# Kernel optimization log

Measured on AMD Instinct MI355X. Metric: run time of the kernel, lower is better.

Reference implementation:

```python
import jax, jax.numpy as jnp
import numpy as np
from jax import lax

T, D, NH, CATS = 1024, 2048, 2048, 1000


def setup_inputs() -> dict:
    key = jax.random.key(0)
    ks = jax.random.split(key, 16)
    s = 0.02
    return {
        "x": jax.random.normal(ks[0], (T, D), dtype=jnp.float32),
        "Wh": jax.random.normal(ks[1], (NH, D), dtype=jnp.float32) * s,
        "Wz": jax.random.normal(ks[2], (NH, D), dtype=jnp.float32) * s,
        "Wr": jax.random.normal(ks[3], (NH, D), dtype=jnp.float32) * s,
        "Uh": jax.random.normal(ks[4], (NH, NH), dtype=jnp.float32) * s,
        "Uz": jax.random.normal(ks[5], (NH, NH), dtype=jnp.float32) * s,
        "bz": jax.random.normal(ks[6], (NH,), dtype=jnp.float32) * s,
        "Ur": jax.random.normal(ks[7], (NH, NH), dtype=jnp.float32) * s,
        "br": jax.random.normal(ks[8], (NH,), dtype=jnp.float32) * s,
        "Wout": jax.random.normal(ks[9], (CATS, NH), dtype=jnp.float32) * s,
        "h0": jax.random.normal(ks[10], (NH,), dtype=jnp.float32),
        "zt0": jax.random.normal(ks[11], (NH,), dtype=jnp.float32),
        "htilde0": jax.random.normal(ks[12], (NH,), dtype=jnp.float32),
        "hprev0": jax.random.normal(ks[13], (NH,), dtype=jnp.float32),
    }


def reference(x, Wh, Wz, Wr, Uh, Uz, bz, Ur, br, Wout, h0, zt0, htilde0, hprev0):
    # Batch the input projections over all timesteps: [T,d] @ [d,nh] -> [T,nh]
    xh = x @ Wh.T
    xz = x @ Wz.T
    xr = x @ Wr.T

    # Faithful to the original update ORDER: h is computed from the *stale*
    # zt/htilde (from the previous iteration), then gates are refreshed.
    # The original's hadamard(a, b) = linear(a, diag(b)) is exactly a * b.
    def step(carry, xs):
        h, zt, htilde, hprev = carry
        xh_t, xz_t, xr_t = xs
        h_new = (1.0 - zt) * hprev + zt * htilde
        zt_new = jax.nn.sigmoid(xz_t + hprev @ Uz.T + bz)
        htilde_new = jnp.tanh(xh_t + hprev @ Uh.T)
        # rt = sigmoid(xr_t + hprev @ Ur.T + br)  # computed in original, never used
        return (h_new, zt_new, htilde_new, h_new), None

    (h_fin, _, _, _), _ = lax.scan(step, (h0, zt0, htilde0, hprev0), (xh, xz, xr))
    logits = h_fin @ Wout.T  # [cats]
    return jax.nn.softmax(logits, axis=0)
```

## Files before the change

### kernel.cpp

```cpp
#include <hip/hip_runtime.h>
#include <math.h>

#define TT  1024
#define DD  2048
#define NHH 2048
#define CC  1000

__global__ void k_init(const float* __restrict__ hp0, unsigned long long* __restrict__ Hbuf) {
    int i = blockIdx.x * blockDim.x + threadIdx.x;
    if (i < NHH) Hbuf[i] = (unsigned long long)__float_as_uint(hp0[i]);
}

__global__ __launch_bounds__(256) void k_gemm(const float* __restrict__ X,
                                              const float* __restrict__ Wh,
                                              const float* __restrict__ Wz,
                                              const float* __restrict__ bz,
                                              float* __restrict__ XH,
                                              float* __restrict__ XZ) {
    __shared__ float As[32][68];
    __shared__ float Bs[32][68];
    const int z = blockIdx.z;
    const float* __restrict__ W = z ? Wz : Wh;
    float* __restrict__ OUT = z ? XZ : XH;
    const int n0 = blockIdx.x * 64;
    const int m0 = blockIdx.y * 64;
    const int tid = threadIdx.x;
    const int tx = tid & 15, ty = tid >> 4;
    const int lr = tid >> 2;
    const int lc = (tid & 3) * 8;

    float acc[4][4] = {};
    for (int k0 = 0; k0 < DD; k0 += 32) {
        float4 a0 = *(const float4*)&X[(size_t)(m0 + lr) * DD + k0 + lc];
        float4 a1 = *(const float4*)&X[(size_t)(m0 + lr) * DD + k0 + lc + 4];
        float4 b0 = *(const float4*)&W[(size_t)(n0 + lr) * DD + k0 + lc];
        float4 b1 = *(const float4*)&W[(size_t)(n0 + lr) * DD + k0 + lc + 4];
        As[lc+0][lr]=a0.x; As[lc+1][lr]=a0.y; As[lc+2][lr]=a0.z; As[lc+3][lr]=a0.w;
        As[lc+4][lr]=a1.x; As[lc+5][lr]=a1.y; As[lc+6][lr]=a1.z; As[lc+7][lr]=a1.w;
        Bs[lc+0][lr]=b0.x; Bs[lc+1][lr]=b0.y; Bs[lc+2][lr]=b0.z; Bs[lc+3][lr]=b0.w;
        Bs[lc+4][lr]=b1.x; Bs[lc+5][lr]=b1.y; Bs[lc+6][lr]=b1.z; Bs[lc+7][lr]=b1.w;
        __syncthreads();
#pragma unroll
        for (int kk = 0; kk < 32; ++kk) {
            float4 av = *(const float4*)&As[kk][ty * 4];
            float4 bv = *(const float4*)&Bs[kk][tx * 4];
            acc[0][0] = fmaf(av.x, bv.x, acc[0][0]); acc[0][1] = fmaf(av.x, bv.y, acc[0][1]);
            acc[0][2] = fmaf(av.x, bv.z, acc[0][2]); acc[0][3] = fmaf(av.x, bv.w, acc[0][3]);
            acc[1][0] = fmaf(av.y, bv.x, acc[1][0]); acc[1][1] = fmaf(av.y, bv.y, acc[1][1]);
            acc[1][2] = fmaf(av.y, bv.z, acc[1][2]); acc[1][3] = fmaf(av.y, bv.w, acc[1][3]);
            acc[2][0] = fmaf(av.z, bv.x, acc[2][0]); acc[2][1] = fmaf(av.z, bv.y, acc[2][1]);
            acc[2][2] = fmaf(av.z, bv.z, acc[2][2]); acc[2][3] = fmaf(av.z, bv.w, acc[2][3]);
            acc[3][0] = fmaf(av.w, bv.x, acc[3][0]); acc[3][1] = fmaf(av.w, bv.y, acc[3][1]);
            acc[3][2] = fmaf(av.w, bv.z, acc[3][2]); acc[3][3] = fmaf(av.w, bv.w, acc[3][3]);
        }
        __syncthreads();
    }
    float4 bias = make_float4(0.f, 0.f, 0.f, 0.f);
    if (z) bias = *(const float4*)&bz[n0 + tx * 4];
#pragma unroll
    for (int i = 0; i < 4; ++i) {
        float4 o = make_float4(acc[i][0] + bias.x, acc[i][1] + bias.y,
                               acc[i][2] + bias.z, acc[i][3] + bias.w);
        *(float4*)&OUT[(size_t)(m0 + ty * 4 + i) * NHH + n0 + tx * 4] = o;
    }
}

__global__ __launch_bounds__(256, 2) void k_recur(
    const float* __restrict__ XH, const float* __restrict__ XZ,
    const float* __restrict__ Uh, const float* __restrict__ Uz,
    const float* __restrict__ zt0, const float* __restrict__ ht0,
    const float* __restrict__ hp0,
    unsigned long long* __restrict__ Hbuf) {
    __shared__ float Hs[NHH];
    __shared__ float zt_s[8], ht_s[8], hpr_s[8], dot_s[16];
    const int tid  = threadIdx.x;
    const int wave = tid >> 6, lane = tid & 63;
    const int base8 = blockIdx.x * 8;

    const float* __restrict__ Um = (wave < 2) ? Uz : Uh;
    const int r0 = base8 + (wave & 1) * 4;
    float u[4][32];
#pragma unroll
    for (int r = 0; r < 4; ++r) {
        const float* __restrict__ row = Um + (size_t)(r0 + r) * NHH;
#pragma unroll
        for (int c = 0; c < 8; ++c) {
            float4 v = *(const float4*)&row[c * 256 + lane * 4];
            u[r][c*4+0] = v.x; u[r][c*4+1] = v.y; u[r][c*4+2] = v.z; u[r][c*4+3] = v.w;
        }
    }
    if (tid < 8) {
        zt_s[tid]  = zt0[base8 + tid];
        ht_s[tid]  = ht0[base8 + tid];
        hpr_s[tid] = hp0[base8 + tid];
    }
    __syncthreads();

    float xzv = 0.f, xhv = 0.f;
    for (int t = 0; t < TT; ++t) {
        if (tid < 8) {
            float zt = zt_s[tid], ht = ht_s[tid], hp = hpr_s[tid];
            float hnew = (1.0f - zt) * hp + zt * ht;
            hpr_s[tid] = hnew;
            unsigned long long pr = ((unsigned long long)(unsigned)(t + 1) << 32)
                                  | (unsigned long long)__float_as_uint(hnew);
            __hip_atomic_store(&Hbuf[(size_t)((t + 1) & 3) * NHH + base8 + tid], pr,
                               __ATOMIC_RELAXED, __HIP_MEMORY_SCOPE_AGENT);
            xzv = XZ[(size_t)t * NHH + base8 + tid];
            xhv = XH[(size_t)t * NHH + base8 + tid];
        }
        const unsigned long long* __restrict__ src = Hbuf + (size_t)(t & 3) * NHH;
        unsigned long long pv[8];
#pragma unroll
        for (int k = 0; k < 8; ++k)
            pv[k] = __hip_atomic_load(&src[k * 256 + tid], __ATOMIC_RELAXED, __HIP_MEMORY_SCOPE_AGENT);
#pragma unroll
        for (int k = 0; k < 8; ++k) {
            while ((unsigned)(pv[k] >> 32) != (unsigned)t) {
                __builtin_amdgcn_s_sleep(1);
                pv[k] = __hip_atomic_load(&src[k * 256 + tid], __ATOMIC_RELAXED, __HIP_MEMORY_SCOPE_AGENT);
            }
            Hs[k * 256 + tid] = __uint_as_float((unsigned)pv[k]);
        }
        __syncthreads();
        float a0 = 0.f, a1 = 0.f, a2 = 0.f, a3 = 0.f;
#pragma unroll
        for (int c = 0; c < 8; ++c) {
            float4 h4 = *(const float4*)&Hs[c * 256 + lane * 4];
            a0 = fmaf(u[0][c*4+0], h4.x, fmaf(u[0][c*4+1], h4.y, fmaf(u[0][c*4+2], h4.z, fmaf(u[0][c*4+3], h4.w, a0))));
            a1 = fmaf(u[1][c*4+0], h4.x, fmaf(u[1][c*4+1], h4.y, fmaf(u[1][c*4+2], h4.z, fmaf(u[1][c*4+3], h4.w, a1))));
            a2 = fmaf(u[2][c*4+0], h4.x, fmaf(u[2][c*4+1], h4.y, fmaf(u[2][c*4+2], h4.z, fmaf(u[2][c*4+3], h4.w, a2))));
            a3 = fmaf(u[3][c*4+0], h4.x, fmaf(u[3][c*4+1], h4.y, fmaf(u[3][c*4+2], h4.z, fmaf(u[3][c*4+3], h4.w, a3))));
        }
#pragma unroll
        for (int off = 32; off > 0; off >>= 1) {
            a0 += __shfl_xor(a0, off);
            a1 += __shfl_xor(a1, off);
            a2 += __shfl_xor(a2, off);
            a3 += __shfl_xor(a3, off);
        }
        if (lane == 0) {
            int di = ((wave & 1) * 4) + ((wave >> 1) * 8);
            dot_s[di + 0] = a0; dot_s[di + 1] = a1; dot_s[di + 2] = a2; dot_s[di + 3] = a3;
        }
        __syncthreads();
        if (tid < 8) {
            zt_s[tid] = 1.0f / (1.0f + expf(-(xzv + dot_s[tid])));
            ht_s[tid] = tanhf(xhv + dot_s[8 + tid]);
        }
        __syncthreads();
    }
}

__global__ __launch_bounds__(256) void k_logits(const unsigned long long* __restrict__ Hbuf,
                                                const float* __restrict__ Wout,
                                                float* __restrict__ lg) {
    __shared__ float Hs[NHH];
    const int tid = threadIdx.x;
    for (int k = tid; k < NHH; k += 256) Hs[k] = __uint_as_float((unsigned)Hbuf[k]);
    __syncthreads();
    const int wave = tid >> 6, lane = tid & 63;
    const int row = blockIdx.x * 4 + wave;
    float a = 0.f;
#pragma unroll
    for (int c = 0; c < 8; ++c) {
        float4 w = *(const float4*)&Wout[(size_t)row * NHH + c * 256 + lane * 4];
        float4 h = *(const float4*)&Hs[c * 256 + lane * 4];
        a = fmaf(w.x, h.x, fmaf(w.y, h.y, fmaf(w.z, h.z, fmaf(w.w, h.w, a))));
    }
#pragma unroll
    for (int off = 32; off > 0; off >>= 1) a += __shfl_xor(a, off);
    if (lane == 0) lg[row] = a;
}

__global__ __launch_bounds__(1024) void k_softmax(const float* __restrict__ lg,
                                                  float* __restrict__ out) {
    const int i = threadIdx.x;
    __shared__ float red[16];
    __shared__ float bc[2];
    float v = (i < CC) ? lg[i] : -3.0e38f;
    float m = v;
#pragma unroll
    for (int off = 32; off > 0; off >>= 1) m = fmaxf(m, __shfl_xor(m, off));
    if ((i & 63) == 0) red[i >> 6] = m;
    __syncthreads();
    if (i == 0) { float mm = red[0]; for (int k = 1; k < 16; ++k) mm = fmaxf(mm, red[k]); bc[0] = mm; }
    __syncthreads();
    float e = (i < CC) ? expf(v - bc[0]) : 0.f;
    float s = e;
#pragma unroll
    for (int off = 32; off > 0; off >>= 1) s += __shfl_xor(s, off);
    if ((i & 63) == 0) red[i >> 6] = s;
    __syncthreads();
    if (i == 0) { float ss = 0.f; for (int k = 0; k < 16; ++k) ss += red[k]; bc[1] = ss; }
    __syncthreads();
    if (i < CC) out[i] = e / bc[1];
}

extern "C" void kernel_launch(void* const* d_in, const int* in_sizes, int n_in,
                              void* d_out, int out_size, void* d_ws, size_t ws_size,
                              hipStream_t stream) {
    const float* x    = (const float*)d_in[0];
    const float* Wh   = (const float*)d_in[1];
    const float* Wz   = (const float*)d_in[2];
    const float* Uh   = (const float*)d_in[4];
    const float* Uz   = (const float*)d_in[5];
    const float* bz   = (const float*)d_in[6];
    const float* Wout = (const float*)d_in[9];
    const float* zt0  = (const float*)d_in[11];
    const float* ht0  = (const float*)d_in[12];
    const float* hp0  = (const float*)d_in[13];
    float* out = (float*)d_out;

    float* XH = (float*)d_ws;
    float* XZ = XH + (size_t)TT * NHH;
    unsigned long long* Hbuf = (unsigned long long*)(XZ + (size_t)TT * NHH);
    float* lg = (float*)(Hbuf + 4 * NHH);

    k_init<<<dim3((NHH + 255) / 256), dim3(256), 0, stream>>>(hp0, Hbuf);
    k_gemm<<<dim3(NHH / 64, TT / 64, 2), dim3(256), 0, stream>>>(x, Wh, Wz, bz, XH, XZ);
    k_recur<<<dim3(256), dim3(256), 0, stream>>>(XH, XZ, Uh, Uz, zt0, ht0, hp0, Hbuf);
    k_logits<<<dim3(250), dim3(256), 0, stream>>>(Hbuf, Wout, lg);
    k_softmax<<<dim3(1), dim3(1024), 0, stream>>>(lg, out);
}
```

Before: 2.195 ms.

## Publish new hidden state right after gates and poll without sleeping

The recurrent kernel now computes the blended hidden state in the same phase as the gate nonlinearities and publishes it to the cross-block exchange buffer immediately. Previously that happened at the top of the next iteration, after an extra barrier. The dot products for step t reuse the shared copy of the previous state, and the spin-wait runs after the publish. It re-polls only the stale entries, with no s_sleep. This moves a barrier and the polling latency off the per-step critical path. The init kernel is dropped and the launch bound is relaxed to one block per SM for more registers. In exchange, busy polling adds memory traffic, and step indexing becomes harder to get right.

```diff
diff --git a/kernel.cpp b/kernel.cpp
--- a/kernel.cpp
+++ b/kernel.cpp
@@ -5,11 +5,6 @@
 #define DD  2048
 #define NHH 2048
 #define CC  1000
-
-__global__ void k_init(const float* __restrict__ hp0, unsigned long long* __restrict__ Hbuf) {
-    int i = blockIdx.x * blockDim.x + threadIdx.x;
-    if (i < NHH) Hbuf[i] = (unsigned long long)__float_as_uint(hp0[i]);
-}
 
 __global__ __launch_bounds__(256) void k_gemm(const float* __restrict__ X,
                                               const float* __restrict__ Wh,
@@ -65,14 +60,14 @@
     }
 }
 
-__global__ __launch_bounds__(256, 2) void k_recur(
+__global__ __launch_bounds__(256, 1) void k_recur(
     const float* __restrict__ XH, const float* __restrict__ XZ,
     const float* __restrict__ Uh, const float* __restrict__ Uz,
     const float* __restrict__ zt0, const float* __restrict__ ht0,
     const float* __restrict__ hp0,
     unsigned long long* __restrict__ Hbuf) {
     __shared__ float Hs[NHH];
-    __shared__ float zt_s[8], ht_s[8], hpr_s[8], dot_s[16];
+    __shared__ float dot_s[16];
     const int tid  = threadIdx.x;
     const int wave = tid >> 6, lane = tid & 63;
     const int base8 = blockIdx.x * 8;
@@ -89,40 +84,30 @@
             u[r][c*4+0] = v.x; u[r][c*4+1] = v.y; u[r][c*4+2] = v.z; u[r][c*4+3] = v.w;
         }
     }
+#pragma unroll
+    for (int k = 0; k < 8; ++k) Hs[k * 256 + tid] = hp0[k * 256 + tid];
+
+    float p_cur = 0.f;
     if (tid < 8) {
-        zt_s[tid]  = zt0[base8 + tid];
-        ht_s[tid]  = ht0[base8 + tid];
-        hpr_s[tid] = hp0[base8 + tid];
-    }
-    __syncthreads();
-
-    float xzv = 0.f, xhv = 0.f;
-    for (int t = 0; t < TT; ++t) {
-        if (tid < 8) {
-            float zt = zt_s[tid], ht = ht_s[tid], hp = hpr_s[tid];
-            float hnew = (1.0f - zt) * hp + zt * ht;
-            hpr_s[tid] = hnew;
-            unsigned long long pr = ((unsigned long long)(unsigned)(t + 1) << 32)
-                                  | (unsigned long long)__float_as_uint(hnew);
-            __hip_atomic_store(&Hbuf[(size_t)((t + 1) & 3) * NHH + base8 + tid], pr,
-                               __ATOMIC_RELAXED, __HIP_MEMORY_SCOPE_AGENT);
-            xzv = XZ[(size_t)t * NHH + base8 + tid];
-            xhv = XH[(size_t)t * NHH + base8 + tid];
-        }
+        float z0 = zt0[base8 + tid], g0 = ht0[base8 + tid], p0 = hp0[base8 + tid];
+        p_cur = (1.0f - z0) * p0 + z0 * g0;
+        unsigned long long pr = (1ull << 32) | (unsigned long long)__float_as_uint(p_cur);
+        __hip_atomic_store(&Hbuf[(size_t)1 * NHH + base8 + tid], pr,
+                           __ATOMIC_RELAXED, __HIP_MEMORY_SCOPE_AGENT);
+    }
+    __syncthreads();
+
+    for (int t = 1; t < TT; ++t) {
         const unsigned long long* __restrict__ src = Hbuf + (size_t)(t & 3) * NHH;
         unsigned long long pv[8];
 #pragma unroll
         for (int k = 0; k < 8; ++k)
             pv[k] = __hip_atomic_load(&src[k * 256 + tid], __ATOMIC_RELAXED, __HIP_MEMORY_SCOPE_AGENT);
-#pragma unroll
-        for (int k = 0; k < 8; ++k) {
-            while ((unsigned)(pv[k] >> 32) != (unsigned)t) {
-                __builtin_amdgcn_s_sleep(1);
-                pv[k] = __hip_atomic_load(&src[k * 256 + tid], __ATOMIC_RELAXED, __HIP_MEMORY_SCOPE_AGENT);
-            }
-            Hs[k * 256 + tid] = __uint_as_float((unsigned)pv[k]);
-        }
-        __syncthreads();
+        float xzv = 0.f, xhv = 0.f;
+        if (tid < 8) {
+            xzv = XZ[(size_t)(t - 1) * NHH + base8 + tid];
+            xhv = XH[(size_t)(t - 1) * NHH + base8 + tid];
+        }
         float a0 = 0.f, a1 = 0.f, a2 = 0.f, a3 = 0.f;
 #pragma unroll
         for (int c = 0; c < 8; ++c) {
@@ -145,9 +130,28 @@
         }
         __syncthreads();
         if (tid < 8) {
-            zt_s[tid] = 1.0f / (1.0f + expf(-(xzv + dot_s[tid])));
-            ht_s[tid] = tanhf(xhv + dot_s[8 + tid]);
-        }
+            float z = 1.0f / (1.0f + expf(-(xzv + dot_s[tid])));
+            float g = tanhf(xhv + dot_s[8 + tid]);
+            float pn = (1.0f - z) * p_cur + z * g;
+            p_cur = pn;
+            unsigned long long pr = ((unsigned long long)(unsigned)(t + 1) << 32)
+                                  | (unsigned long long)__float_as_uint(pn);
+            __hip_atomic_store(&Hbuf[(size_t)((t + 1) & 3) * NHH + base8 + tid], pr,
+                               __ATOMIC_RELAXED, __HIP_MEMORY_SCOPE_AGENT);
+        }
+        for (;;) {
+            unsigned stale = 0;
+#pragma unroll
+            for (int k = 0; k < 8; ++k)
+                if ((unsigned)(pv[k] >> 32) != (unsigned)t) stale |= (1u << k);
+            if (!stale) break;
+#pragma unroll
+            for (int k = 0; k < 8; ++k)
+                if (stale & (1u << k))
+                    pv[k] = __hip_atomic_load(&src[k * 256 + tid], __ATOMIC_RELAXED, __HIP_MEMORY_SCOPE_AGENT);
+        }
+#pragma unroll
+        for (int k = 0; k < 8; ++k) Hs[k * 256 + tid] = __uint_as_float((unsigned)pv[k]);
         __syncthreads();
     }
 }
@@ -217,7 +221,6 @@
     unsigned long long* Hbuf = (unsigned long long*)(XZ + (size_t)TT * NHH);
     float* lg = (float*)(Hbuf + 4 * NHH);
 
-    k_init<<<dim3((NHH + 255) / 256), dim3(256), 0, stream>>>(hp0, Hbuf);
     k_gemm<<<dim3(NHH / 64, TT / 64, 2), dim3(256), 0, stream>>>(x, Wh, Wz, bz, XH, XZ);
     k_recur<<<dim3(256), dim3(256), 0, stream>>>(XH, XZ, Uh, Uz, zt0, ht0, hp0, Hbuf);
     k_logits<<<dim3(250), dim3(256), 0, stream>>>(Hbuf, Wout, lg);
```

After: 2.044 ms. 6.9% less time.
